# Performance work log

Measured on AMD Instinct MI355X. Metric: run time of the kernel, lower is better.

The kernel has to match this reference:

```python
import jax, jax.numpy as jnp
import numpy as np

N_NODES = 10000
N_EDGES = 80000
D = 512
L = 5
ALPHA = 0.1  # LeakyReLU slope inside GraphAttention
ACT_ALPHA = 0.1  # outer activation slope
EPS = 1e-5
W_SCALE = 0.05  # ~ xavier_normal gain 1.414 for fan_in+fan_out=1536


def leaky(x, a):
    return jnp.where(x >= 0, x, a * x)


def setup_inputs() -> dict:
    key = jax.random.key(0)
    ks = jax.random.split(key, 9)
    return {
        "node_feats": jax.random.normal(ks[0], (N_NODES, D), jnp.float32),
        "edge_feats": jax.random.normal(ks[1], (N_EDGES, D), jnp.float32),
        "src": jax.random.randint(ks[2], (N_EDGES,), 0, N_NODES, jnp.int32),
        "dst": jax.random.randint(ks[3], (N_EDGES,), 0, N_NODES, jnp.int32),
        "Wa": jax.random.normal(ks[4], (L, 2 * D, D), jnp.float32) * W_SCALE,
        "Wn": jax.random.normal(ks[5], (L, 2 * D, D), jnp.float32) * W_SCALE,
        "We": jax.random.normal(ks[6], (L, 2 * D, D), jnp.float32) * W_SCALE,
        "Wnc": jax.random.normal(ks[7], (D, 55), jnp.float32) * W_SCALE,
        "Wec": jax.random.normal(ks[8], (D, 2), jnp.float32) * W_SCALE,
    }


def reference(node_feats, edge_feats, src, dst, Wa, Wn, We, Wnc, Wec):
    n = node_feats.shape[0]
    nx, ex = node_feats, edge_feats
    for l in range(L):
        nx_src = nx[src]  # [E, D]
        nx_dst = nx[dst]  # [E, D]
        # a_p = exp(fa([e_x, dst_x]) - columnwise max over edges)
        ap = jnp.concatenate((ex, nx_dst), axis=1) @ Wa[l]
        ap = jnp.exp(ap - jnp.max(ap, axis=0, keepdims=True))
        # a_r = exp(fa([e_x, src_x]) - columnwise max over edges)
        ar = jnp.concatenate((ex, nx_src), axis=1) @ Wa[l]
        ar = jnp.exp(ar - jnp.max(ar, axis=0, keepdims=True))
        # softmax-like normalization per destination node
        z = jax.ops.segment_sum(ap, dst, num_segments=n)  # [N, D]
        a = ap / (z[dst] + EPS)
        # aggregate a * edge_x to destination nodes
        z2 = jax.ops.segment_sum(a * ex, dst, num_segments=n)  # [N, D]
        ft = jnp.concatenate((z2, nx), axis=1) @ Wn[l]
        # edge update: blend src/dst node feats by a_r/a_p shares
        a_sum = ap + ar
        blend = (ar / a_sum) * nx_src + (ap / a_sum) * nx_dst
        ex_new = jnp.concatenate((blend, ex), axis=1) @ We[l]
        # inner leaky_relu then outer activation (both LeakyReLU)
        nx = leaky(leaky(ft, ALPHA), ACT_ALPHA)
        ex = leaky(leaky(ex_new, ALPHA), ACT_ALPHA)
    node_conf = nx @ Wnc
    edge_conf = ex @ Wec
    return (nx, node_conf, ex, edge_conf)
```

## Files before the change

### kernel.cpp

```cpp
#include <hip/hip_runtime.h>
#include <hip/hip_fp16.h>
#include <math.h>

#define D 512
#define NNODES 10000
#define NEDGES 80000
#define LAYERS 5
#define EPS 1e-5f

typedef _Float16 f16x8 __attribute__((ext_vector_type(8)));
typedef float f32x4 __attribute__((ext_vector_type(4)));

__device__ inline unsigned short f2h(float x) { return __half_as_ushort(__float2half(x)); }
__device__ inline float h2f(unsigned short u) { return __half2float(__ushort_as_half(u)); }
__device__ inline uint4 pack8(const unsigned short* v) {
  uint4 r;
  r.x = (unsigned)v[0] | ((unsigned)v[1] << 16);
  r.y = (unsigned)v[2] | ((unsigned)v[3] << 16);
  r.z = (unsigned)v[4] | ((unsigned)v[5] << 16);
  r.w = (unsigned)v[6] | ((unsigned)v[7] << 16);
  return r;
}
__device__ inline void unpack8(uint4 v, unsigned short* o) {
  o[0] = v.x & 0xffff; o[1] = v.x >> 16;
  o[2] = v.y & 0xffff; o[3] = v.y >> 16;
  o[4] = v.z & 0xffff; o[5] = v.z >> 16;
  o[6] = v.w & 0xffff; o[7] = v.w >> 16;
}

__device__ inline void gload16(const void* g, void* l) {
  __builtin_amdgcn_global_load_lds((const __attribute__((address_space(1))) void*)g,
                                   (__attribute__((address_space(3))) void*)l, 16, 0, 0);
}

__device__ inline int octA(int r, int o) {
  return ((o >> 2) << 6) + ((((o & 3) ^ ((r >> 1) & 3))) << 4);
}

__global__ __launch_bounds__(256) void toF16_k(const float* __restrict__ src,
                                               char* __restrict__ dst, int nOct) {
  for (long long i = (long long)blockIdx.x * 256 + threadIdx.x; i < nOct;
       i += (long long)gridDim.x * 256) {
    int row = (int)(i >> 6), oct = (int)(i & 63);
    const float* s = src + (size_t)row * 512 + oct * 8;
    float4 x0 = *(const float4*)s, x1 = *(const float4*)(s + 4);
    float xs[8] = {x0.x, x0.y, x0.z, x0.w, x1.x, x1.y, x1.z, x1.w};
    unsigned short h[8];
#pragma unroll
    for (int j = 0; j < 8; j++) h[j] = f2h(xs[j]);
    *(uint4*)(dst + (size_t)row * 1024 + octA(row, oct)) = pack8(h);
  }
}

__global__ __launch_bounds__(256) void wprep_k(const float* __restrict__ Wa,
                                               const float* __restrict__ Wn,
                                               const float* __restrict__ We,
                                               char* __restrict__ WT) {
  __shared__ float tile[64][65];
  int mat = blockIdx.z;
  const float* W = (mat < 5) ? Wa + (size_t)mat * 1024 * 512
                 : (mat < 10) ? Wn + (size_t)(mat - 5) * 1024 * 512
                              : We + (size_t)(mat - 10) * 1024 * 512;
  char* out = WT + (size_t)mat * 512 * 2048;
  int n0 = blockIdx.x * 64, k0 = blockIdx.y * 64;
  int t = threadIdx.x;
  int ty = t >> 2, tx = t & 3;
  const float* wr = W + (size_t)(k0 + ty) * 512 + n0 + tx * 16;
  float4 v0 = *(const float4*)(wr + 0), v1 = *(const float4*)(wr + 4);
  float4 v2 = *(const float4*)(wr + 8), v3 = *(const float4*)(wr + 12);
  float vv[16] = {v0.x, v0.y, v0.z, v0.w, v1.x, v1.y, v1.z, v1.w,
                  v2.x, v2.y, v2.z, v2.w, v3.x, v3.y, v3.z, v3.w};
#pragma unroll
  for (int j = 0; j < 16; j++) tile[ty][tx * 16 + j] = vv[j];
  __syncthreads();
#pragma unroll
  for (int p = 0; p < 2; p++) {
    int chunk = t + p * 256;
    int n = chunk >> 3, cc = chunk & 7;
    float xs[8];
#pragma unroll
    for (int j = 0; j < 8; j++) xs[j] = tile[cc * 8 + j][n];
    unsigned short h[8];
#pragma unroll
    for (int j = 0; j < 8; j++) h[j] = f2h(xs[j]);
    int ng = n0 + n;
    int kc = (k0 >> 3) + cc;
    *(uint4*)(out + (size_t)ng * 2048 + octA(ng, kc)) = pack8(h);
  }
}

__global__ __launch_bounds__(256) void hist_k(const int* __restrict__ dst, int* __restrict__ cnt) {
  int e = blockIdx.x * 256 + threadIdx.x;
  if (e < NEDGES) atomicAdd(&cnt[dst[e]], 1);
}

__global__ __launch_bounds__(256) void scan_k(const int* __restrict__ cnt,
                                              int* __restrict__ off, int* __restrict__ cur) {
  __shared__ int part[256];
  const int CH = (NNODES + 255) / 256;
  int t = threadIdx.x;
  int s = 0;
  int l0 = t * CH;
  for (int i = 0; i < CH; i++) {
    int idx = l0 + i;
    if (idx < NNODES) s += cnt[idx];
  }
  part[t] = s;
  __syncthreads();
  if (t == 0) {
    int acc = 0;
    for (int i = 0; i < 256; i++) { int v = part[i]; part[i] = acc; acc += v; }
  }
  __syncthreads();
  int acc = part[t];
  for (int i = 0; i < CH; i++) {
    int idx = l0 + i;
    if (idx < NNODES) { off[idx] = acc; cur[idx] = acc; acc += cnt[idx]; }
  }
  if (t == 255) off[NNODES] = acc;
}

__global__ __launch_bounds__(256) void scatter_k(const int* __restrict__ dst,
                                                 int* __restrict__ cur, int* __restrict__ eid) {
  int e = blockIdx.x * 256 + threadIdx.x;
  if (e < NEDGES) {
    int p = atomicAdd(&cur[dst[e]], 1);
    eid[p] = e;
  }
}

template<int KT, bool ACT, bool OUT_I, bool CMAX>
__global__ __launch_bounds__(256) void gemmI(const char* __restrict__ X1,
                                             const char* __restrict__ X2,
                                             const char* __restrict__ BW, int cb0,
                                             void* __restrict__ Yout, int R,
                                             const int* __restrict__ srcI,
                                             const int* __restrict__ dstI,
                                             const float* __restrict__ Na,
                                             float* __restrict__ part_p,
                                             float* __restrict__ part_r) {
  __shared__ char smem[32768];
  const int tid = threadIdx.x;
  const int lane = tid & 63, wv = tid >> 6;
  int flat = blockIdx.y * 4 + blockIdx.x;
  int total = gridDim.y * 4;
  int xcd = flat & 7, idx = flat >> 3;
  int q = total >> 3, rem = total & 7;
  int base = xcd * q + (xcd < rem ? xcd : rem);
  int f2 = base + idx;
  const int bn0 = (f2 & 3) * 128, bm0 = (f2 >> 2) * 128;
  const int r16 = lane & 15, g = lane >> 4;
  const int mo = (wv >> 1) * 64, no = (wv & 1) * 64;
  const int lr16 = lane >> 2, ls16 = (lane & 3) * 16;
  f32x4 acc[4][4];
#pragma unroll
  for (int i = 0; i < 4; i++)
#pragma unroll
    for (int j = 0; j < 4; j++) acc[i][j] = (f32x4){0.f, 0.f, 0.f, 0.f};

  int offA[4], offB[4];
#pragma unroll
  for (int mi = 0; mi < 4; mi++) {
    int row = mo + mi * 16 + r16;
    offA[mi] = row * 64 + ((g ^ ((row >> 1) & 3)) << 4);
  }
#pragma unroll
  for (int ni = 0; ni < 4; ni++) {
    int row = no + ni * 16 + r16;
    offB[ni] = row * 64 + ((g ^ ((row >> 1) & 3)) << 4);
  }

  const char* pA0;
  const char* pA1;
  const char* pB0;
  const char* pB1;
  {
    int g0 = bm0 + wv * 16 + lr16; if (g0 > R - 1) g0 = R - 1;
    int g1 = bm0 + (4 + wv) * 16 + lr16; if (g1 > R - 1) g1 = R - 1;
    pA0 = X1 + (size_t)g0 * 1024 + ls16;
    pA1 = X1 + (size_t)g1 * 1024 + ls16;
    int n0r = bn0 + wv * 16 + lr16;
    int n1r = bn0 + (4 + wv) * 16 + lr16;
    pB0 = BW + (size_t)n0r * 2048 + cb0 * 16 + ls16;
    pB1 = BW + (size_t)n1r * 2048 + cb0 * 16 + ls16;
  }

#define STAGE(buf)                                              \
  {                                                             \
    char* sb = smem + (buf) * 16384;                            \
    gload16(pA0, sb + wv * 1024);                               \
    gload16(pA1, sb + (4 + wv) * 1024);                         \
    gload16(pB0, sb + 8192 + wv * 1024);                        \
    gload16(pB1, sb + 8192 + (4 + wv) * 1024);                  \
    pA0 += 64; pA1 += 64; pB0 += 64; pB1 += 64;                 \
  }

  STAGE(0);
  __syncthreads();
  int cur = 0;
  for (int kt = 0; kt < KT; kt += 32) {
    if (kt + 32 < KT) {
      if (KT == 1024 && kt + 32 == 512) {
        int g0 = bm0 + wv * 16 + lr16; if (g0 > R - 1) g0 = R - 1;
        int g1 = bm0 + (4 + wv) * 16 + lr16; if (g1 > R - 1) g1 = R - 1;
        pA0 = X2 + (size_t)g0 * 1024 + ls16;
        pA1 = X2 + (size_t)g1 * 1024 + ls16;
      }
      STAGE(cur ^ 1);
    }
    const char* As = smem + cur * 16384;
    const char* Bs = As + 8192;
    f16x8 a[4], b[4];
#pragma unroll
    for (int mi = 0; mi < 4; mi++) a[mi] = *(const f16x8*)(As + offA[mi]);
#pragma unroll
    for (int ni = 0; ni < 4; ni++) b[ni] = *(const f16x8*)(Bs + offB[ni]);
#pragma unroll
    for (int mi = 0; mi < 4; mi++)
#pragma unroll
      for (int ni = 0; ni < 4; ni++)
        acc[mi][ni] = __builtin_amdgcn_mfma_f32_16x16x32_f16(a[mi], b[ni], acc[mi][ni], 0, 0, 0);
    __syncthreads();
    cur ^= 1;
  }
#undef STAGE

  if (!OUT_I) {
    float* Y = (float*)Yout;
#pragma unroll
    for (int mi = 0; mi < 4; mi++)
#pragma unroll
      for (int j = 0; j < 4; j++) {
        int row = bm0 + mo + mi * 16 + g * 4 + j;
        if (row < R) {
#pragma unroll
          for (int ni = 0; ni < 4; ni++) {
            float v = acc[mi][ni][j];
            if (ACT) v = (v >= 0.f) ? v : 0.01f * v;
            Y[(size_t)row * 512 + bn0 + no + ni * 16 + r16] = v;
          }
        }
      }
  } else {
    float* stg = (float*)smem;
    const int rg = tid >> 5, cq = (tid & 31) * 4;
    float4 mp4 = make_float4(-1e30f, -1e30f, -1e30f, -1e30f);
    float4 mr4 = mp4;
#pragma unroll
    for (int h = 0; h < 2; h++) {
      __syncthreads();
      if ((wv >> 1) == h) {
#pragma unroll
        for (int mi = 0; mi < 4; mi++)
#pragma unroll
          for (int j = 0; j < 4; j++) {
            int rl = mi * 16 + g * 4 + j;
#pragma unroll
            for (int ni = 0; ni < 4; ni++) {
              float v = acc[mi][ni][j];
              if (ACT) v = (v >= 0.f) ? v : 0.01f * v;
              stg[rl * 128 + no + ni * 16 + r16] = v;
            }
          }
      }
      __syncthreads();
#pragma unroll
      for (int qq = 0; qq < 4; qq++) {
        int idx2 = tid + qq * 256;
        int rl = idx2 >> 4, oc = idx2 & 15;
        int grow = bm0 + h * 64 + rl;
        if (grow < R) {
          unsigned short hh[8];
#pragma unroll
          for (int j = 0; j < 8; j++) hh[j] = f2h(stg[rl * 128 + oc * 8 + j]);
          int oct = (bn0 >> 3) + oc;
          *(uint4*)((char*)Yout + (size_t)grow * 1024 + octA(grow, oct)) = pack8(hh);
        }
      }
      if (CMAX) {
#pragma unroll 2
        for (int r = rg * 8; r < rg * 8 + 8; r++) {
          int grow = bm0 + h * 64 + r;
          int d = dstI[grow], s = srcI[grow];
          float4 v = *(const float4*)&stg[r * 128 + cq];
          v.x = h2f(f2h(v.x)); v.y = h2f(f2h(v.y));
          v.z = h2f(f2h(v.z)); v.w = h2f(f2h(v.w));
          float4 nd = *(const float4*)&Na[(size_t)d * 512 + bn0 + cq];
          float4 ns = *(const float4*)&Na[(size_t)s * 512 + bn0 + cq];
          mp4.x = fmaxf(mp4.x, v.x + nd.x); mp4.y = fmaxf(mp4.y, v.y + nd.y);
          mp4.z = fmaxf(mp4.z, v.z + nd.z); mp4.w = fmaxf(mp4.w, v.w + nd.w);
          mr4.x = fmaxf(mr4.x, v.x + ns.x); mr4.y = fmaxf(mr4.y, v.y + ns.y);
          mr4.z = fmaxf(mr4.z, v.z + ns.z); mr4.w = fmaxf(mr4.w, v.w + ns.w);
        }
      }
    }
    if (CMAX) {
      __syncthreads();
      float* red = (float*)smem;
      *(float4*)&red[rg * 128 + cq] = mp4;
      *(float4*)&red[1024 + rg * 128 + cq] = mr4;
      __syncthreads();
      if (tid < 128) {
        float vp = -1e30f, vr = -1e30f;
#pragma unroll
        for (int gi = 0; gi < 8; gi++) {
          vp = fmaxf(vp, red[gi * 128 + tid]);
          vr = fmaxf(vr, red[1024 + gi * 128 + tid]);
        }
        int panel = f2 >> 2;
        part_p[(size_t)panel * 512 + bn0 + tid] = vp;
        part_r[(size_t)panel * 512 + bn0 + tid] = vr;
      }
    }
  }
}

__global__ __launch_bounds__(256) void colmax_red_k(const float* __restrict__ part,
                                                    float* __restrict__ m) {
  int idx = blockIdx.x * 256 + threadIdx.x;
  int c = idx & 511;
  const float* P = part + (size_t)(idx >> 9) * (625 * 512) + c;
  float v = -1e30f;
#pragma unroll 1
  for (int b = 0; b < 625; b += 5) {
    float v0 = P[(size_t)(b + 0) * 512], v1 = P[(size_t)(b + 1) * 512];
    float v2 = P[(size_t)(b + 2) * 512], v3 = P[(size_t)(b + 3) * 512];
    float v4 = P[(size_t)(b + 4) * 512];
    v = fmaxf(v, fmaxf(fmaxf(v0, v1), fmaxf(fmaxf(v2, v3), v4)));
  }
  m[idx] = v;
}

__global__ __launch_bounds__(256) void aggblend_k(const char* __restrict__ EaH,
                                                  const float* __restrict__ Na,
                                                  const char* __restrict__ exI,
                                                  const char* __restrict__ nxI,
                                                  const int* __restrict__ src,
                                                  const int* __restrict__ off,
                                                  const int* __restrict__ eid,
                                                  const float* __restrict__ mp,
                                                  const float* __restrict__ mr,
                                                  char* __restrict__ blendH,
                                                  char* __restrict__ z2I) {
  const int w = threadIdx.x >> 6, o = threadIdx.x & 63;
  int n = blockIdx.x * 4 + w;
  if (n >= NNODES) return;
  float m_p[8], m_r[8], nd[8], xd[8], z[8], z2[8];
#pragma unroll
  for (int j = 0; j < 8; j++) {
    m_p[j] = mp[o * 8 + j];
    m_r[j] = mr[o * 8 + j];
    z[j] = 0.f; z2[j] = 0.f;
  }
  {
    const float* np = Na + (size_t)n * 512 + o * 8;
    float4 d0 = *(const float4*)np, d1 = *(const float4*)(np + 4);
    nd[0] = d0.x; nd[1] = d0.y; nd[2] = d0.z; nd[3] = d0.w;
    nd[4] = d1.x; nd[5] = d1.y; nd[6] = d1.z; nd[7] = d1.w;
    unsigned short hh[8];
    unpack8(*(const uint4*)(nxI + (size_t)n * 1024 + octA(n, o)), hh);
#pragma unroll
    for (int j = 0; j < 8; j++) xd[j] = h2f(hh[j]);
  }
  const int i0 = off[n], i1 = off[n + 1];
  if (i0 < i1) {
    int e = eid[i0];
    int s = src[e];
    uint4 cea = *(const uint4*)(EaH + (size_t)e * 1024 + octA(e, o));
    const float* ns = Na + (size_t)s * 512 + o * 8;
    float4 cs0 = *(const float4*)ns, cs1 = *(const float4*)(ns + 4);
    uint4 cx = *(const uint4*)(exI + (size_t)e * 1024 + octA(e, o));
    uint4 cn = *(const uint4*)(nxI + (size_t)s * 1024 + octA(s, o));
    for (int i = i0; i < i1; i++) {
      int en = 0, sn = 0;
      float4 ps0, ps1;
      uint4 pea, px, pn;
      const bool more = (i + 1 < i1);
      if (more) {
        en = eid[i + 1];
        sn = src[en];
        pea = *(const uint4*)(EaH + (size_t)en * 1024 + octA(en, o));
        const float* ns2 = Na + (size_t)sn * 512 + o * 8;
        ps0 = *(const float4*)ns2; ps1 = *(const float4*)(ns2 + 4);
        px = *(const uint4*)(exI + (size_t)en * 1024 + octA(en, o));
        pn = *(const uint4*)(nxI + (size_t)sn * 1024 + octA(sn, o));
      }
      unsigned short eh[8], xh[8], sh[8];
      unpack8(cea, eh);
      unpack8(cx, xh);
      unpack8(cn, sh);
      float sv[8] = {cs0.x, cs0.y, cs0.z, cs0.w, cs1.x, cs1.y, cs1.z, cs1.w};
      unsigned short bh[8];
#pragma unroll
      for (int j = 0; j < 8; j++) {
        float ev = h2f(eh[j]);
        float sp = ev + nd[j] - m_p[j];
        float sr = ev + sv[j] - m_r[j];
        float ap = __expf(sp);
        float xe = h2f(xh[j]);
        z[j] += ap;
        z2[j] += ap * xe;
        float u = sr - sp;
        float evx = __expf(-fabsf(u));
        float wpos = 1.f / (1.f + evx);
        float wr = (u >= 0.f) ? wpos : 1.f - wpos;
        float xs_ = h2f(sh[j]);
        bh[j] = f2h(wr * xs_ + (1.f - wr) * xd[j]);
      }
      *(uint4*)(blendH + (size_t)e * 1024 + octA(e, o)) = pack8(bh);
      if (more) {
        e = en; s = sn;
        cea = pea; cs0 = ps0; cs1 = ps1;
        cx = px; cn = pn;
      }
    }
  }
  unsigned short zh[8];
#pragma unroll
  for (int j = 0; j < 8; j++) zh[j] = f2h(z2[j] / (z[j] + EPS));
  *(uint4*)(z2I + (size_t)n * 1024 + octA(n, o)) = pack8(zh);
}

__global__ __launch_bounds__(256) void nodeconf_k(const float* __restrict__ nx,
                                                  const float* __restrict__ Wnc,
                                                  float* __restrict__ out) {
  int w = threadIdx.x >> 6, lane = threadIdx.x & 63;
  int n = blockIdx.x * 4 + w;
  const float* r = nx + (size_t)n * D;
  if (lane < 55) {
    float acc = 0.f;
    for (int k = 0; k < D; k++) acc = fmaf(r[k], Wnc[k * 55 + lane], acc);
    out[(size_t)n * 55 + lane] = acc;
  }
}

__global__ __launch_bounds__(256) void edgeconf_k(const float* __restrict__ ex,
                                                  const float* __restrict__ Wec,
                                                  float* __restrict__ out) {
  int w = threadIdx.x >> 6, lane = threadIdx.x & 63;
  int e = blockIdx.x * 4 + w;
  const float* r = ex + (size_t)e * D;
  float a0 = 0.f, a1 = 0.f;
#pragma unroll
  for (int j = 0; j < 8; j++) {
    int c = lane + j * 64;
    float x = r[c];
    a0 = fmaf(x, Wec[c * 2 + 0], a0);
    a1 = fmaf(x, Wec[c * 2 + 1], a1);
  }
#pragma unroll
  for (int off = 32; off; off >>= 1) {
    a0 += __shfl_down(a0, off);
    a1 += __shfl_down(a1, off);
  }
  if (lane == 0) { out[(size_t)e * 2 + 0] = a0; out[(size_t)e * 2 + 1] = a1; }
}

extern "C" void kernel_launch(void* const* d_in, const int* in_sizes, int n_in,
                              void* d_out, int out_size, void* d_ws, size_t ws_size,
                              hipStream_t stream) {
  const float* in_nx = (const float*)d_in[0];
  const float* in_ex = (const float*)d_in[1];
  const int* src = (const int*)d_in[2];
  const int* dst = (const int*)d_in[3];
  const float* Wa = (const float*)d_in[4];
  const float* Wn = (const float*)d_in[5];
  const float* We = (const float*)d_in[6];
  const float* Wnc = (const float*)d_in[7];
  const float* Wec = (const float*)d_in[8];

  float* out = (float*)d_out;
  float* o_nx = out;
  float* o_nc = o_nx + (size_t)NNODES * D;
  float* o_ex = o_nc + (size_t)NNODES * 55;
  float* o_ec = o_ex + (size_t)NEDGES * D;

  const size_t SZ_EH = (size_t)NEDGES * 1024;
  const size_t SZ_NH = (size_t)NNODES * 1024;
  const size_t SZ_NF = (size_t)NNODES * 2048;
  const size_t MATSZ = (size_t)512 * 2048;
  char* w = (char*)d_ws;
  char* EaH = w;
  char* blendH = w + SZ_EH;
  char* exA = w + 2 * SZ_EH;
  char* nxA = w + 3 * SZ_EH;
  float* Na = (float*)(w + 3 * SZ_EH + SZ_NH);
  char* z2I = w + 3 * SZ_EH + SZ_NH + SZ_NF;
  float* mpf = (float*)(w + 3 * SZ_EH + 2 * SZ_NH + SZ_NF);
  char* WT = w + 3 * SZ_EH + 2 * SZ_NH + SZ_NF + 8192;
  char* csr = WT + 15 * MATSZ;
  int* cnt = (int*)csr;
  int* offp = cnt + NNODES + 8;
  int* cur = offp + NNODES + 8;
  int* eid = cur + NNODES + 8;
  float* part_p = (float*)(eid + NEDGES);
  float* part_r = part_p + 625 * 512;

  char* exB = (char*)o_ex;
  char* nxB = (char*)o_nx;

  wprep_k<<<dim3(8, 16, 15), 256, 0, stream>>>(Wa, Wn, We, WT);
  toF16_k<<<2048, 256, 0, stream>>>(in_ex, exA, NEDGES * 64);
  toF16_k<<<2048, 256, 0, stream>>>(in_nx, nxA, NNODES * 64);
  hipMemsetAsync(cnt, 0, NNODES * sizeof(int), stream);
  hist_k<<<(NEDGES + 255) / 256, 256, 0, stream>>>(dst, cnt);
  scan_k<<<1, 256, 0, stream>>>(cnt, offp, cur);
  scatter_k<<<(NEDGES + 255) / 256, 256, 0, stream>>>(dst, cur, eid);

  dim3 gE(4, NEDGES / 128);
  dim3 gN(4, (NNODES + 127) / 128);

  for (int l = 0; l < LAYERS; l++) {
    const char* WaT = WT + (size_t)l * MATSZ;
    const char* WnT = WT + (size_t)(5 + l) * MATSZ;
    const char* WeT = WT + (size_t)(10 + l) * MATSZ;
    char* exCur = (l & 1) ? exB : exA;
    char* exNxt = (l & 1) ? exA : exB;
    char* nxCur = (l & 1) ? nxB : nxA;
    char* nxNxt = (l & 1) ? nxA : nxB;

    gemmI<512, false, false, false><<<gN, 256, 0, stream>>>(
        nxCur, nullptr, WaT, 64, Na, NNODES, nullptr, nullptr, nullptr, nullptr, nullptr);
    gemmI<512, false, true, true><<<gE, 256, 0, stream>>>(
        exCur, nullptr, WaT, 0, EaH, NEDGES, src, dst, Na, part_p, part_r);

    colmax_red_k<<<4, 256, 0, stream>>>(part_p, mpf);

    aggblend_k<<<(NNODES + 3) / 4, 256, 0, stream>>>(EaH, Na, exCur, nxCur, src,
                                                     offp, eid, mpf, mpf + 512, blendH, z2I);

    if (l < 4)
      gemmI<1024, true, true, false><<<gN, 256, 0, stream>>>(
          z2I, nxCur, WnT, 0, nxNxt, NNODES, nullptr, nullptr, nullptr, nullptr, nullptr);
    else
      gemmI<1024, true, false, false><<<gN, 256, 0, stream>>>(
          z2I, nxCur, WnT, 0, o_nx, NNODES, nullptr, nullptr, nullptr, nullptr, nullptr);

    if (l < 4)
      gemmI<1024, true, true, false><<<gE, 256, 0, stream>>>(
          blendH, exCur, WeT, 0, exNxt, NEDGES, nullptr, nullptr, nullptr, nullptr, nullptr);
    else
      gemmI<1024, true, false, false><<<gE, 256, 0, stream>>>(
          blendH, exCur, WeT, 0, o_ex, NEDGES, nullptr, nullptr, nullptr, nullptr, nullptr);
  }

  nodeconf_k<<<NNODES / 4, 256, 0, stream>>>(o_nx, Wnc, o_nc);
  edgeconf_k<<<NEDGES / 4, 256, 0, stream>>>(o_ex, Wec, o_ec);
}
```

Before: 2.151 ms.

## Triple-buffer GEMM K-loop with explicit vmcnt waits and MFMA priority boost

Moves the gemmI main loop from double to triple-buffered LDS staging. Two tiles are prefetched ahead and completion is tracked with s_waitcnt vmcnt plus a single barrier per iteration instead of two __syncthreads. MFMA sections are raised in priority with s_setprio. The aim is to hide global-load latency better, at the cost of 48KB of LDS per block, which may reduce occupancy.

```diff
diff --git a/kernel.cpp b/kernel.cpp
--- a/kernel.cpp
+++ b/kernel.cpp
@@ -139,9 +139,10 @@
                                              const float* __restrict__ Na,
                                              float* __restrict__ part_p,
                                              float* __restrict__ part_r) {
-  __shared__ char smem[32768];
+  __shared__ char smem[49152];
   const int tid = threadIdx.x;
   const int lane = tid & 63, wv = tid >> 6;
+  const int NT = KT / 32;
   int flat = blockIdx.y * 4 + blockIdx.x;
   int total = gridDim.y * 4;
   int xcd = flat & 7, idx = flat >> 3;
@@ -185,43 +186,50 @@
     pB1 = BW + (size_t)n1r * 2048 + cb0 * 16 + ls16;
   }
 
-#define STAGE(buf)                                              \
+  int us = 0;
+#define STAGE()                                                 \
   {                                                             \
-    char* sb = smem + (buf) * 16384;                            \
+    char* sb = smem + (us % 3) * 16384;                         \
     gload16(pA0, sb + wv * 1024);                               \
     gload16(pA1, sb + (4 + wv) * 1024);                         \
     gload16(pB0, sb + 8192 + wv * 1024);                        \
     gload16(pB1, sb + 8192 + (4 + wv) * 1024);                  \
     pA0 += 64; pA1 += 64; pB0 += 64; pB1 += 64;                 \
-  }
-
-  STAGE(0);
-  __syncthreads();
-  int cur = 0;
-  for (int kt = 0; kt < KT; kt += 32) {
-    if (kt + 32 < KT) {
-      if (KT == 1024 && kt + 32 == 512) {
+    us++;                                                       \
+  }
+
+  STAGE();
+  STAGE();
+  for (int t = 0; t < NT; ++t) {
+    if (t + 1 < NT) {
+      asm volatile("s_waitcnt vmcnt(4)" ::: "memory");
+    } else {
+      asm volatile("s_waitcnt vmcnt(0)" ::: "memory");
+    }
+    __builtin_amdgcn_s_barrier();
+    if (us < NT) {
+      if (KT == 1024 && us == 16) {
         int g0 = bm0 + wv * 16 + lr16; if (g0 > R - 1) g0 = R - 1;
         int g1 = bm0 + (4 + wv) * 16 + lr16; if (g1 > R - 1) g1 = R - 1;
         pA0 = X2 + (size_t)g0 * 1024 + ls16;
         pA1 = X2 + (size_t)g1 * 1024 + ls16;
       }
-      STAGE(cur ^ 1);
+      STAGE();
     }
-    const char* As = smem + cur * 16384;
+    const char* As = smem + (t % 3) * 16384;
     const char* Bs = As + 8192;
     f16x8 a[4], b[4];
 #pragma unroll
     for (int mi = 0; mi < 4; mi++) a[mi] = *(const f16x8*)(As + offA[mi]);
 #pragma unroll
     for (int ni = 0; ni < 4; ni++) b[ni] = *(const f16x8*)(Bs + offB[ni]);
+    __builtin_amdgcn_s_setprio(1);
 #pragma unroll
     for (int mi = 0; mi < 4; mi++)
 #pragma unroll
       for (int ni = 0; ni < 4; ni++)
         acc[mi][ni] = __builtin_amdgcn_mfma_f32_16x16x32_f16(a[mi], b[ni], acc[mi][ni], 0, 0, 0);
-    __syncthreads();
-    cur ^= 1;
+    __builtin_amdgcn_s_setprio(0);
   }
 #undef STAGE
 
```

Measured after the change: 2.080 ms. 1.03x faster.
